# Kernel optimization log

Measured on AMD Instinct MI355X. Metric: run time of the kernel, lower is better.

Reference implementation:

```python
import jax, jax.numpy as jnp
import numpy as np

DIM = 512
NUM_HEADS = 8
HEAD_DIM = DIM // NUM_HEADS
SCALE = HEAD_DIM ** -0.5


def setup_inputs() -> dict:
    key = jax.random.key(0)
    k_x, k_qkv, k_proj, k_pb = jax.random.split(key, 4)
    x = jax.random.normal(k_x, (2, 4096, DIM), dtype=jnp.float32)
    # nn.Linear weights: stored as [out, in]; qkv_bias=False so no qkv bias.
    w_qkv = jax.random.normal(k_qkv, (3 * DIM, DIM), dtype=jnp.float32) * (DIM ** -0.5)
    w_proj = jax.random.normal(k_proj, (DIM, DIM), dtype=jnp.float32) * (DIM ** -0.5)
    b_proj = jax.random.normal(k_pb, (DIM,), dtype=jnp.float32) * 0.01
    return {"x": x, "w_qkv": w_qkv, "w_proj": w_proj, "b_proj": b_proj}


def reference(x, w_qkv, w_proj, b_proj):
    B, N, D = x.shape
    H, Hd = NUM_HEADS, HEAD_DIM
    # qkv: [B, N, 3D] -> [3, B, H, N, Hd]
    qkv = (x @ w_qkv.T).reshape(B, N, 3, H, Hd).transpose(2, 0, 3, 1, 4)
    q, k, v = qkv[0], qkv[1], qkv[2]
    # Naive full attention matrix in fp32 (matches original non-fused path).
    attn = jnp.einsum('bhqd,bhkd->bhqk', q, k) * SCALE
    attn = jax.nn.softmax(attn, axis=-1)
    out = jnp.einsum('bhqk,bhkd->bhqd', attn, v)
    out = out.transpose(0, 2, 1, 3).reshape(B, N, D)
    return out @ w_proj.T + b_proj
```

## Files before the change

### kernel.cpp

```cpp
#include <hip/hip_runtime.h>
#include <stdint.h>

#define SEQ   4096
#define DIMM  512
#define HDIM  64
#define NH    8
#define ROWS  8192
#define QKVN  1536

typedef __attribute__((ext_vector_type(8))) __bf16 bf16x8;
typedef __attribute__((ext_vector_type(4))) __bf16 bf16x4;
typedef __attribute__((ext_vector_type(4))) float  f32x4;
typedef __attribute__((ext_vector_type(4))) short  s16x4;
typedef __attribute__((ext_vector_type(2))) uint32_t u32x2;

__device__ __forceinline__ uint32_t cvtpk(float lo, float hi) {
  uint32_t w;
  asm("v_cvt_pk_bf16_f32 %0, %1, %2" : "=v"(w) : "v"(lo), "v"(hi));
  return w;
}

__device__ __forceinline__ f32x4 mfma16(bf16x8 a, bf16x8 b, f32x4 c) {
  return __builtin_amdgcn_mfma_f32_16x16x32_bf16(a, b, c, 0, 0, 0);
}

__device__ __forceinline__ f32x4 pv_mfma(s16x4 a, s16x4 b, f32x4 c) {
#if __has_builtin(__builtin_amdgcn_mfma_f32_16x16x16bf16_1k)
  return __builtin_amdgcn_mfma_f32_16x16x16bf16_1k(a, b, c, 0, 0, 0);
#elif __has_builtin(__builtin_amdgcn_mfma_f32_16x16x16_bf16)
  return __builtin_amdgcn_mfma_f32_16x16x16_bf16(
      __builtin_bit_cast(bf16x4, a), __builtin_bit_cast(bf16x4, b), c, 0, 0, 0);
#else
  f32x4 d = c;
  asm volatile("v_mfma_f32_16x16x16_bf16 %0, %1, %2, %3"
               : "=v"(d) : "v"(a), "v"(b), "0"(d));
  return d;
#endif
}

#if __has_builtin(__builtin_amdgcn_exp2f)
#define EXP2F(x) __builtin_amdgcn_exp2f(x)
#else
#define EXP2F(x) exp2f(x)
#endif

__device__ __forceinline__ void gld16(const void* g, void* l) {
  __builtin_amdgcn_global_load_lds(
      (const __attribute__((address_space(1))) uint32_t*)g,
      (__attribute__((address_space(3))) uint32_t*)l, 16, 0, 0);
}

#define X4  (ROWS * DIMM / 4)
#define Q4  (QKVN * DIMM / 4)
#define P4  (DIMM * DIMM / 4)

__global__ __launch_bounds__(256) void cvt_kernel(
    const float* __restrict__ x, const float* __restrict__ wq,
    const float* __restrict__ wp, uint16_t* __restrict__ xb,
    uint16_t* __restrict__ wqb, uint16_t* __restrict__ wpb) {
  int idx = blockIdx.x * 256 + threadIdx.x;
  const float* src; uint16_t* dst; int i4;
  if (idx < X4)            { src = x;  dst = xb;  i4 = idx; }
  else if (idx < X4 + Q4)  { src = wq; dst = wqb; i4 = idx - X4; }
  else                     { src = wp; dst = wpb; i4 = idx - X4 - Q4; }
  float4 v = ((const float4*)src)[i4];
  uint2 o;
  o.x = cvtpk(v.x, v.y);
  o.y = cvtpk(v.z, v.w);
  ((uint2*)dst)[i4] = o;
}

__device__ __forceinline__ void gemm_core(
    const uint16_t* __restrict__ A, const uint16_t* __restrict__ B,
    uint16_t (*As)[128 * 32], uint16_t (*Bs)[128 * 32], f32x4 acc[4][4]) {
  const int tid = threadIdx.x;
  const int lane = tid & 63, wave = tid >> 6;
  const int quad = lane >> 4, l16 = lane & 15;
  const int wr = (wave & 1) * 64, wc = (wave >> 1) * 64;
  const int bm = blockIdx.x, bn = blockIdx.y;
  const int sw = (l16 >> 1) & 3;

  auto stage = [&](int buf, int kt) {
#pragma unroll
    for (int it = 0; it < 2; ++it) {
      int L = it * 256 + tid;
      int r = L >> 2, c = L & 3;
      int gc = c ^ ((r >> 1) & 3);
      int ldsoff = (it * 256 + (tid & ~63)) * 16;
      gld16((const char*)A + ((size_t)(bm * 128 + r) * DIMM + kt * 32) * 2 + gc * 16,
            (char*)As[buf] + ldsoff);
      gld16((const char*)B + ((size_t)(bn * 128 + r) * DIMM + kt * 32) * 2 + gc * 16,
            (char*)Bs[buf] + ldsoff);
    }
  };

  stage(0, 0);
  for (int kt = 0; kt < DIMM / 32; ++kt) {
    const int cur = kt & 1;
    __syncthreads();
    if (kt < DIMM / 32 - 1) stage(cur ^ 1, kt + 1);

    bf16x8 af[4], bfr[4];
#pragma unroll
    for (int i = 0; i < 4; ++i)
      af[i] = *(const bf16x8*)(As[cur] + (wr + i * 16 + l16) * 32 + ((quad ^ sw) * 8));
#pragma unroll
    for (int j = 0; j < 4; ++j)
      bfr[j] = *(const bf16x8*)(Bs[cur] + (wc + j * 16 + l16) * 32 + ((quad ^ sw) * 8));
    __builtin_amdgcn_s_setprio(1);
#pragma unroll
    for (int i = 0; i < 4; ++i)
#pragma unroll
      for (int j = 0; j < 4; ++j)
        acc[i][j] = mfma16(af[i], bfr[j], acc[i][j]);
    __builtin_amdgcn_s_setprio(0);
  }
}

__global__ __launch_bounds__(256, 4) void qkv_gemm(
    const uint16_t* __restrict__ xb, const uint16_t* __restrict__ wqb,
    uint16_t* __restrict__ qd, uint16_t* __restrict__ kd,
    uint16_t* __restrict__ vt) {
  __shared__ __align__(16) uint16_t As[2][128 * 32];
  __shared__ __align__(16) uint16_t Bs[2][128 * 32];
  f32x4 acc[4][4];
#pragma unroll
  for (int i = 0; i < 4; ++i)
#pragma unroll
    for (int j = 0; j < 4; ++j) acc[i][j] = f32x4{0.f, 0.f, 0.f, 0.f};

  gemm_core(xb, wqb, As, Bs, acc);

  const int lane = threadIdx.x & 63, wave = threadIdx.x >> 6;
  const int quad = lane >> 4, l16 = lane & 15;
  const int wr = (wave & 1) * 64, wc = (wave >> 1) * 64;
  const float qscale = 0.125f * 1.44269504f;
#pragma unroll
  for (int i = 0; i < 4; ++i) {
    int m0 = blockIdx.x * 128 + wr + i * 16 + quad * 4;
    int b = m0 >> 12, n0 = m0 & 4095;
#pragma unroll
    for (int j = 0; j < 4; ++j) {
      int jc = blockIdx.y * 128 + wc + j * 16 + l16;
      int region = jc >> 9;
      int h = (jc >> 6) & 7, hd = jc & 63;
      int bh = (b << 3) | h;
      if (region == 0) {
        uint32_t w01 = cvtpk(acc[i][j][0] * qscale, acc[i][j][1] * qscale);
        uint32_t w23 = cvtpk(acc[i][j][2] * qscale, acc[i][j][3] * qscale);
        size_t rb = ((size_t)bh * SEQ + n0) * HDIM + hd;
        qd[rb]            = (uint16_t)w01;
        qd[rb + HDIM]     = (uint16_t)(w01 >> 16);
        qd[rb + 2 * HDIM] = (uint16_t)w23;
        qd[rb + 3 * HDIM] = (uint16_t)(w23 >> 16);
      } else if (region == 1) {
        uint32_t w01 = cvtpk(acc[i][j][0], acc[i][j][1]);
        uint32_t w23 = cvtpk(acc[i][j][2], acc[i][j][3]);
        size_t rb = ((size_t)bh * SEQ + n0) * HDIM + hd;
        kd[rb]            = (uint16_t)w01;
        kd[rb + HDIM]     = (uint16_t)(w01 >> 16);
        kd[rb + 2 * HDIM] = (uint16_t)w23;
        kd[rb + 3 * HDIM] = (uint16_t)(w23 >> 16);
      } else {
        uint2 pk;
        pk.x = cvtpk(acc[i][j][0], acc[i][j][1]);
        pk.y = cvtpk(acc[i][j][2], acc[i][j][3]);
        *(uint2*)(vt + ((size_t)bh * HDIM + hd) * SEQ + n0) = pk;
      }
    }
  }
}

__global__ __launch_bounds__(512, 4) void attn_kernel(
    const uint16_t* __restrict__ qd, const uint16_t* __restrict__ kd,
    const uint16_t* __restrict__ vt, uint16_t* __restrict__ ao) {
  __shared__ __align__(16) uint16_t Ks[2][128 * 64];
  __shared__ __align__(16) uint16_t Vs[2][64 * 128];

  const int tid = threadIdx.x, lane = tid & 63, wave = tid >> 6;
  const int quad = lane >> 4, l16 = lane & 15;
  const int pair = wave >> 1, khalf = wave & 1;
  const int wid = blockIdx.x;
  const int xcd = wid & 7, slot = wid >> 3;
  const int bh = xcd + 8 * (slot & 1);
  const int qt = slot >> 1;
  const size_t base_qk = (size_t)bh * SEQ * HDIM;
  const size_t base_v  = (size_t)bh * HDIM * SEQ;
  const int sw7 = l16 & 7;

  auto stage = [&](int buf, int kt) {
#pragma unroll
    for (int it = 0; it < 2; ++it) {
      int L = it * 512 + tid;
      int ldsoff = (it * 512 + (tid & ~63)) * 16;
      int rk = L >> 3, ck = L & 7;
      int gck = ck ^ (rk & 7);
      gld16((const char*)kd + (base_qk + (size_t)(kt * 128 + rk) * HDIM) * 2 + gck * 16,
            (char*)Ks[buf] + ldsoff);
      int rv = L >> 4, cv = L & 15;
      int gcv = cv ^ (rv & 15);
      gld16((const char*)vt + (base_v + (size_t)rv * SEQ + (size_t)kt * 128) * 2 + gcv * 16,
            (char*)Vs[buf] + ldsoff);
    }
  };

  bf16x8 qf[2][2];
#pragma unroll
  for (int it2 = 0; it2 < 2; ++it2)
#pragma unroll
    for (int kh = 0; kh < 2; ++kh)
      qf[it2][kh] = *(const bf16x8*)(qd + base_qk +
          (size_t)(qt * 128 + pair * 32 + it2 * 16 + l16) * HDIM + kh * 32 + quad * 8);

  f32x4 O[2][4];
  float lsum[2] = {0.f, 0.f};
#pragma unroll
  for (int a = 0; a < 2; ++a)
#pragma unroll
    for (int d = 0; d < 4; ++d) O[a][d] = f32x4{0.f, 0.f, 0.f, 0.f};

  stage(0, 0);
  for (int kt = 0; kt < SEQ / 128; ++kt) {
    const int cur = kt & 1;
    __syncthreads();
    if (kt < SEQ / 128 - 1) stage(cur ^ 1, kt + 1);

    bf16x8 kf[4][2];
#pragma unroll
    for (int jh = 0; jh < 4; ++jh) {
      int jf = khalf * 4 + jh;
      const uint16_t* krow = Ks[cur] + (jf * 16 + l16) * 64;
      kf[jh][0] = *(const bf16x8*)(krow + ((quad ^ sw7) * 8));
      kf[jh][1] = *(const bf16x8*)(krow + (((4 + quad) ^ sw7) * 8));
    }

#pragma unroll
    for (int jh = 0; jh < 4; ++jh) {
      f32x4 P[2];
      __builtin_amdgcn_s_setprio(1);
#pragma unroll
      for (int it2 = 0; it2 < 2; ++it2) {
        f32x4 s = f32x4{0.f, 0.f, 0.f, 0.f};
        s = mfma16(kf[jh][0], qf[it2][0], s);
        s = mfma16(kf[jh][1], qf[it2][1], s);
        P[it2] = s;
      }
      __builtin_amdgcn_s_setprio(0);

      s16x4 pb[2];
#pragma unroll
      for (int it2 = 0; it2 < 2; ++it2) {
        float p0 = EXP2F(P[it2][0]);
        float p1 = EXP2F(P[it2][1]);
        float p2 = EXP2F(P[it2][2]);
        float p3 = EXP2F(P[it2][3]);
        lsum[it2] += (p0 + p1) + (p2 + p3);
        u32x2 t;
        t.x = cvtpk(p0, p1);
        t.y = cvtpk(p2, p3);
        pb[it2] = __builtin_bit_cast(s16x4, t);
      }

      s16x4 va[4];
#pragma unroll
      for (int dl = 0; dl < 4; ++dl)
        va[dl] = *(const s16x4*)((const char*)Vs[cur] + (dl * 16 + l16) * 256 +
                  (((8 * khalf + 2 * jh + (quad >> 1)) ^ l16) & 15) * 16 +
                  (quad & 1) * 8);
      __builtin_amdgcn_s_setprio(1);
#pragma unroll
      for (int it2 = 0; it2 < 2; ++it2)
#pragma unroll
        for (int dl = 0; dl < 4; ++dl)
          O[it2][dl] = pv_mfma(va[dl], pb[it2], O[it2][dl]);
      __builtin_amdgcn_s_setprio(0);
    }
  }

  __syncthreads();
  if (!(wave & 1)) {
    f32x4* ob = (f32x4*)((char*)Ks + pair * 8192);
#pragma unroll
    for (int it2 = 0; it2 < 2; ++it2)
#pragma unroll
      for (int dl = 0; dl < 4; ++dl)
        ob[(it2 * 4 + dl) * 64 + lane] = O[it2][dl];
    float2* lb = (float2*)((char*)Vs + pair * 512);
    lb[lane] = make_float2(lsum[0], lsum[1]);
  }
  __syncthreads();
  if (wave & 1) {
    const f32x4* ob = (const f32x4*)((char*)Ks + pair * 8192);
    float2 lp = ((const float2*)((char*)Vs + pair * 512))[lane];
    lsum[0] += lp.x; lsum[1] += lp.y;
#pragma unroll
    for (int it2 = 0; it2 < 2; ++it2)
#pragma unroll
      for (int dl = 0; dl < 4; ++dl)
        O[it2][dl] += ob[(it2 * 4 + dl) * 64 + lane];

    const int b = bh >> 3, h = bh & 7;
#pragma unroll
    for (int it2 = 0; it2 < 2; ++it2) {
      float l = lsum[it2];
      l += __shfl_xor(l, 16);
      l += __shfl_xor(l, 32);
      float inv = 1.0f / l;
      int q = qt * 128 + pair * 32 + it2 * 16 + l16;
      size_t rowbase = ((size_t)(b * SEQ + q)) * DIMM + h * HDIM;
#pragma unroll
      for (int dl = 0; dl < 4; ++dl) {
        uint2 pk;
        pk.x = cvtpk(O[it2][dl][0] * inv, O[it2][dl][1] * inv);
        pk.y = cvtpk(O[it2][dl][2] * inv, O[it2][dl][3] * inv);
        *(uint2*)(ao + rowbase + dl * 16 + quad * 4) = pk;
      }
    }
  }
}

__global__ __launch_bounds__(256, 4) void proj_gemm(
    const uint16_t* __restrict__ ao, const uint16_t* __restrict__ wpb,
    const float* __restrict__ bprj, float* __restrict__ out) {
  __shared__ __align__(16) uint16_t As[2][128 * 32];
  __shared__ __align__(16) uint16_t Bs[2][128 * 32];
  f32x4 acc[4][4];
#pragma unroll
  for (int i = 0; i < 4; ++i)
#pragma unroll
    for (int j = 0; j < 4; ++j) acc[i][j] = f32x4{0.f, 0.f, 0.f, 0.f};

  gemm_core(ao, wpb, As, Bs, acc);

  const int lane = threadIdx.x & 63, wave = threadIdx.x >> 6;
  const int quad = lane >> 4, l16 = lane & 15;
  const int wr = (wave & 1) * 64, wc = (wave >> 1) * 64;
#pragma unroll
  for (int i = 0; i < 4; ++i) {
    int m0 = blockIdx.x * 128 + wr + i * 16 + quad * 4;
#pragma unroll
    for (int j = 0; j < 4; ++j) {
      int jc = blockIdx.y * 128 + wc + j * 16 + l16;
      float bias = bprj[jc];
#pragma unroll
      for (int r = 0; r < 4; ++r)
        out[(size_t)(m0 + r) * DIMM + jc] = acc[i][j][r] + bias;
    }
  }
}

extern "C" void kernel_launch(void* const* d_in, const int* in_sizes, int n_in,
                              void* d_out, int out_size, void* d_ws, size_t ws_size,
                              hipStream_t stream) {
  const float* x     = (const float*)d_in[0];
  const float* wqkv  = (const float*)d_in[1];
  const float* wproj = (const float*)d_in[2];
  const float* bproj = (const float*)d_in[3];

  char* ws = (char*)d_ws;
  uint16_t* xb  = (uint16_t*)(ws + 0);
  uint16_t* wqb = (uint16_t*)(ws + 8388608);
  uint16_t* wpb = (uint16_t*)(ws + 9961472);
  uint16_t* qd  = (uint16_t*)(ws + 10485760);
  uint16_t* kd  = (uint16_t*)(ws + 18874368);
  uint16_t* vt  = (uint16_t*)(ws + 27262976);
  uint16_t* ao  = (uint16_t*)(ws + 35651584);

  cvt_kernel<<<(X4 + Q4 + P4) / 256, 256, 0, stream>>>(x, wqkv, wproj, xb, wqb, wpb);
  qkv_gemm<<<dim3(64, 12), 256, 0, stream>>>(xb, wqb, qd, kd, vt);
  attn_kernel<<<512, 512, 0, stream>>>(qd, kd, vt, ao);
  proj_gemm<<<dim3(64, 4), 256, 0, stream>>>(ao, wpb, bproj, (float*)d_out);
}
```

Before: 192.8 us.

## Use 16x16x32 MFMA for PV via permlane swaps to build K=32 P fragments

Replaces the PV product's 16x16x16 bf16 MFMAs with 16x16x32 MFMAs, halving the number of PV matrix instructions. To do this it computes all score tiles for the 128-key block first, then uses v_permlane32/16_swap to rearrange the packed bf16 probabilities from pairs of 16-key tiles into K=32 operand fragments. V is read as 16-byte bf16x8 loads instead of 8-byte ones. This costs extra register pressure from holding all P tiles at once, adds permlane instructions, and relies on the swap pattern matching the MFMA operand layout.

After: 183.4 us. 1.05x faster.

```diff
diff --git a/kernel.cpp b/kernel.cpp
--- a/kernel.cpp
+++ b/kernel.cpp
@@ -9,10 +9,8 @@
 #define QKVN  1536
 
 typedef __attribute__((ext_vector_type(8))) __bf16 bf16x8;
-typedef __attribute__((ext_vector_type(4))) __bf16 bf16x4;
 typedef __attribute__((ext_vector_type(4))) float  f32x4;
-typedef __attribute__((ext_vector_type(4))) short  s16x4;
-typedef __attribute__((ext_vector_type(2))) uint32_t u32x2;
+typedef __attribute__((ext_vector_type(4))) uint32_t u32x4;
 
 __device__ __forceinline__ uint32_t cvtpk(float lo, float hi) {
   uint32_t w;
@@ -20,22 +18,15 @@
   return w;
 }
 
+__device__ __forceinline__ void swap32(uint32_t& a, uint32_t& b) {
+  asm("v_permlane32_swap_b32 %0, %1" : "+v"(a), "+v"(b));
+}
+__device__ __forceinline__ void swap16(uint32_t& a, uint32_t& b) {
+  asm("v_permlane16_swap_b32 %0, %1" : "+v"(a), "+v"(b));
+}
+
 __device__ __forceinline__ f32x4 mfma16(bf16x8 a, bf16x8 b, f32x4 c) {
   return __builtin_amdgcn_mfma_f32_16x16x32_bf16(a, b, c, 0, 0, 0);
-}
-
-__device__ __forceinline__ f32x4 pv_mfma(s16x4 a, s16x4 b, f32x4 c) {
-#if __has_builtin(__builtin_amdgcn_mfma_f32_16x16x16bf16_1k)
-  return __builtin_amdgcn_mfma_f32_16x16x16bf16_1k(a, b, c, 0, 0, 0);
-#elif __has_builtin(__builtin_amdgcn_mfma_f32_16x16x16_bf16)
-  return __builtin_amdgcn_mfma_f32_16x16x16_bf16(
-      __builtin_bit_cast(bf16x4, a), __builtin_bit_cast(bf16x4, b), c, 0, 0, 0);
-#else
-  f32x4 d = c;
-  asm volatile("v_mfma_f32_16x16x16_bf16 %0, %1, %2, %3"
-               : "=v"(d) : "v"(a), "v"(b), "0"(d));
-  return d;
-#endif
 }
 
 #if __has_builtin(__builtin_amdgcn_exp2f)
@@ -234,45 +225,59 @@
       kf[jh][1] = *(const bf16x8*)(krow + (((4 + quad) ^ sw7) * 8));
     }
 
-#pragma unroll
-    for (int jh = 0; jh < 4; ++jh) {
-      f32x4 P[2];
-      __builtin_amdgcn_s_setprio(1);
+    f32x4 P[4][2];
+    __builtin_amdgcn_s_setprio(1);
+#pragma unroll
+    for (int jh = 0; jh < 4; ++jh)
 #pragma unroll
       for (int it2 = 0; it2 < 2; ++it2) {
         f32x4 s = f32x4{0.f, 0.f, 0.f, 0.f};
         s = mfma16(kf[jh][0], qf[it2][0], s);
         s = mfma16(kf[jh][1], qf[it2][1], s);
-        P[it2] = s;
-      }
-      __builtin_amdgcn_s_setprio(0);
-
-      s16x4 pb[2];
+        P[jh][it2] = s;
+      }
+    __builtin_amdgcn_s_setprio(0);
+
+    uint32_t sp[4][2][2];
+#pragma unroll
+    for (int jh = 0; jh < 4; ++jh)
 #pragma unroll
       for (int it2 = 0; it2 < 2; ++it2) {
-        float p0 = EXP2F(P[it2][0]);
-        float p1 = EXP2F(P[it2][1]);
-        float p2 = EXP2F(P[it2][2]);
-        float p3 = EXP2F(P[it2][3]);
+        float p0 = EXP2F(P[jh][it2][0]);
+        float p1 = EXP2F(P[jh][it2][1]);
+        float p2 = EXP2F(P[jh][it2][2]);
+        float p3 = EXP2F(P[jh][it2][3]);
         lsum[it2] += (p0 + p1) + (p2 + p3);
-        u32x2 t;
-        t.x = cvtpk(p0, p1);
-        t.y = cvtpk(p2, p3);
-        pb[it2] = __builtin_bit_cast(s16x4, t);
-      }
-
-      s16x4 va[4];
+        sp[jh][it2][0] = cvtpk(p0, p1);
+        sp[jh][it2][1] = cvtpk(p2, p3);
+      }
+
+    bf16x8 pb[2][2];
+#pragma unroll
+    for (int kp = 0; kp < 2; ++kp)
+#pragma unroll
+      for (int it2 = 0; it2 < 2; ++it2) {
+        uint32_t t0 = sp[2 * kp][it2][0], t2 = sp[2 * kp + 1][it2][0];
+        swap32(t0, t2); swap16(t0, t2);
+        uint32_t t1 = sp[2 * kp][it2][1], t3 = sp[2 * kp + 1][it2][1];
+        swap32(t1, t3); swap16(t1, t3);
+        u32x4 w = {t0, t1, t2, t3};
+        pb[kp][it2] = __builtin_bit_cast(bf16x8, w);
+      }
+
+#pragma unroll
+    for (int kp = 0; kp < 2; ++kp) {
+      bf16x8 va[4];
 #pragma unroll
       for (int dl = 0; dl < 4; ++dl)
-        va[dl] = *(const s16x4*)((const char*)Vs[cur] + (dl * 16 + l16) * 256 +
-                  (((8 * khalf + 2 * jh + (quad >> 1)) ^ l16) & 15) * 16 +
-                  (quad & 1) * 8);
+        va[dl] = *(const bf16x8*)((const char*)Vs[cur] + (dl * 16 + l16) * 256 +
+                                  (((khalf * 8 + kp * 4 + quad) ^ l16) & 15) * 16);
       __builtin_amdgcn_s_setprio(1);
 #pragma unroll
       for (int it2 = 0; it2 < 2; ++it2)
 #pragma unroll
         for (int dl = 0; dl < 4; ++dl)
-          O[it2][dl] = pv_mfma(va[dl], pb[it2], O[it2][dl]);
+          O[it2][dl] = mfma16(va[dl], pb[kp][it2], O[it2][dl]);
       __builtin_amdgcn_s_setprio(0);
     }
   }
```
